# Kernel optimization log

Measured on AMD Instinct MI355X. Metric: run time of the kernel, lower is better.

Reference implementation:

```python
import math
import jax, jax.numpy as jnp
import numpy as np

B, N, C, H = 4, 1025, 768, 12
D = C // H                      # head_dim = 64
SCALE = D ** -0.5
NUM = N // 4                    # CSA block size = 256
FUSE_T = math.ceil(0.1 * (N - 1))     # 103
ENH_T = math.ceil(0.1 * (N - 1))      # 103


def _csa_mask():
    # has_cls=True: tokens 1..4*NUM get block id 0..3; cls (idx 0) gets -1 (unmasked).
    bid = (jnp.arange(N) - 1) // NUM
    same = (bid[:, None] == bid[None, :]) & (bid[:, None] >= 0) & (bid[:, None] < 4)
    return jnp.where(same, -jnp.inf, 0.0).astype(jnp.float32)  # [N, N]


def setup_inputs() -> dict:
    key = jax.random.key(0)
    kx, kq, kw, kb = jax.random.split(key, 4)
    x = jax.random.normal(kx, (B, N, C), dtype=jnp.float32)
    w_qkv = jax.random.normal(kq, (3 * C, C), dtype=jnp.float32) * 0.02  # Linear(C, 3C, bias=False)
    w_out = jax.random.normal(kw, (C, C), dtype=jnp.float32) * 0.02
    b_out = jax.random.normal(kb, (C,), dtype=jnp.float32) * 0.02
    return {"x": x, "w_qkv": w_qkv, "w_out": w_out, "b_out": b_out}


def reference(x, w_qkv, w_out, b_out):
    b, n, c = x.shape
    h, d = H, c // H
    # qkv projection + rearrange 'b n (qkv h d) -> qkv b h n d'
    qkv = (x @ w_qkv.T).reshape(b, n, 3, h, d).transpose(2, 0, 3, 1, 4)
    q, k, v = qkv[0], qkv[1], qkv[2]          # each [b, h, n, d]

    scores = jnp.einsum('bhxd,bhyd->bhxy', q, k) * SCALE + _csa_mask()
    att = jax.nn.softmax(scores, axis=-1)     # [b, h, n, n]  (dropout=0, eval)

    ctx = jnp.einsum('bhxy,bhyd->bhxd', att, v)
    out = ctx.transpose(0, 2, 1, 3).reshape(b, n, c) @ w_out.T + b_out

    # cls-attention-driven token selection
    cls_attn = att[:, :, 0, 1:].mean(axis=1)  # [b, n-1]
    _, fuse_idx = jax.lax.top_k(-cls_attn, FUSE_T)   # smallest, ascending
    _, enh_idx = jax.lax.top_k(cls_attn, ENH_T)      # largest, descending
    fuse_index = jnp.broadcast_to(fuse_idx[:, :, None], (b, FUSE_T, c))
    enhance_index = jnp.broadcast_to(enh_idx[:, :, None], (b, ENH_T, c))
    return (out, enhance_index, enh_idx, fuse_index, fuse_idx, cls_attn)
```

## Files before the change

kernel.cpp:

```cpp
#include <hip/hip_runtime.h>


#define B_  4
#define N_  1025
#define C_  768
#define H_  12
#define D_  64
#define M_TOT (B_ * N_)
#define M_PAD 4224
#define KEXP 2304
#define NPAD 1088

#define OFF_EIND 3148800
#define OFF_EIDX 3465216
#define OFF_FIND 3465628
#define OFF_FIDX 3782044
#define OFF_CLS  3782456

#define WS_F64   0
#define WS_XS    196608
#define WS_QKVB  5062656
#define WS_OUTB  7716864
#define WS_QE    8601600
#define WS_KE    11943936
#define WS_VT    15286272

#define DQ0 0
#define DMS 3072
#define DLG 39936
#define DMX 89136
#define DZ  89184
#define DMV 89232

#define SPLIT_A_ITEMS (M_PAD * 192)
#define SPLIT_B1_ITEMS (2304 * 192)
#define SPLIT_B2_ITEMS (768 * 192)
#define SPLIT_TOTAL (SPLIT_A_ITEMS + SPLIT_B1_ITEMS + SPLIT_B2_ITEMS)

typedef short s16x8 __attribute__((ext_vector_type(8)));
typedef float f32x4 __attribute__((ext_vector_type(4)));

__device__ inline unsigned short f2bf(float f) {
    unsigned u = __float_as_uint(f);
    u += 0x7FFF + ((u >> 16) & 1);
    return (unsigned short)(u >> 16);
}
__device__ inline float bf2f(unsigned short h) {
    return __uint_as_float(((unsigned)h) << 16);
}

__device__ __forceinline__ void gl2lds16(const unsigned short* g, unsigned short* l) {
    __builtin_amdgcn_global_load_lds(
        (const __attribute__((address_space(1))) unsigned int*)g,
        (__attribute__((address_space(3))) unsigned int*)l,
        16, 0, 0);
}

__device__ inline void gemm_decode(int lid, int NT, int& m, int& n) {
    int gi = lid / (8 * NT);
    int r  = lid % (8 * NT);
    int base = gi * 8;
    int gsize = (33 - base < 8) ? (33 - base) : 8;
    n = r / gsize;
    m = base + r % gsize;
}

__global__ __launch_bounds__(256) void split_all_kernel(
    const float* __restrict__ x, const float* __restrict__ w_qkv,
    const float* __restrict__ w_out,
    unsigned short* __restrict__ xs, unsigned short* __restrict__ qkvB,
    unsigned short* __restrict__ outB)
{
    int idx = blockIdx.x * 256 + threadIdx.x;
    if (idx < SPLIT_A_ITEMS) {
        int m = idx / 192, c4 = (idx - m * 192) * 4;
        ushort4 hi = make_ushort4(0,0,0,0), lo = hi;
        if (m < M_TOT) {
            float4 f = *(const float4*)&x[(size_t)m * C_ + c4];
            hi.x = f2bf(f.x); hi.y = f2bf(f.y); hi.z = f2bf(f.z); hi.w = f2bf(f.w);
            lo.x = f2bf(f.x - bf2f(hi.x)); lo.y = f2bf(f.y - bf2f(hi.y));
            lo.z = f2bf(f.z - bf2f(hi.z)); lo.w = f2bf(f.w - bf2f(hi.w));
        }
        unsigned short* d = xs + (size_t)m * KEXP + c4;
        *(ushort4*)(d)        = hi;
        *(ushort4*)(d + 768)  = hi;
        *(ushort4*)(d + 1536) = lo;
        return;
    }
    idx -= SPLIT_A_ITEMS;
    const float* src;
    unsigned short* dst;
    if (idx < SPLIT_B1_ITEMS) { src = w_qkv; dst = qkvB; }
    else { idx -= SPLIT_B1_ITEMS; if (idx >= SPLIT_B2_ITEMS) return; src = w_out; dst = outB; }
    int m = idx / 192, c4 = (idx - m * 192) * 4;
    float4 f = *(const float4*)&src[(size_t)m * C_ + c4];
    ushort4 hi, lo;
    hi.x = f2bf(f.x); hi.y = f2bf(f.y); hi.z = f2bf(f.z); hi.w = f2bf(f.w);
    lo.x = f2bf(f.x - bf2f(hi.x)); lo.y = f2bf(f.y - bf2f(hi.y));
    lo.z = f2bf(f.z - bf2f(hi.z)); lo.w = f2bf(f.w - bf2f(hi.w));
    unsigned short* d = dst + (size_t)m * KEXP + c4;
    *(ushort4*)(d)        = hi;
    *(ushort4*)(d + 768)  = lo;
    *(ushort4*)(d + 1536) = hi;
}

__global__ __launch_bounds__(256) void gemm_qkv_kernel(
    const unsigned short* __restrict__ A, const unsigned short* __restrict__ Bm,
    unsigned short* __restrict__ qe, unsigned short* __restrict__ ke,
    unsigned short* __restrict__ vtp)
{
    __shared__ unsigned short AsF[3*4096];
    __shared__ unsigned short BsF[3*4096];
    int mi, ni;
    gemm_decode(blockIdx.x, 18, mi, ni);
    const int n0 = ni * 128;
    const int m0 = mi * 128;
    const int t = threadIdx.x;
    const int lane = t & 63, wv = t >> 6;
    const int wr = wv >> 1, wc = wv & 1;
    const int q4 = lane >> 4, r = lane & 15;
    const int lrr = lane >> 2;
    const int lcc = ((lane & 3) ^ ((lane >> 3) & 3)) * 8;
    const int sw  = (q4 ^ ((r >> 1) & 3)) * 8;

    f32x4 acc[4][4];
    #pragma unroll
    for (int i = 0; i < 4; i++)
        #pragma unroll
        for (int j = 0; j < 4; j++)
            #pragma unroll
            for (int e = 0; e < 4; e++) acc[i][j][e] = 0.f;

    const unsigned short* gA = A  + (size_t)(m0 + wv*16 + lrr) * KEXP + lcc;
    const unsigned short* gB = Bm + (size_t)(n0 + wv*16 + lrr) * KEXP + lcc;

    auto STAGE = [&](int kt, int o) {
        const unsigned short* a = gA + kt * 32;
        const unsigned short* b = gB + kt * 32;
        gl2lds16(a,                       AsF + o + wv*512);
        gl2lds16(a + (size_t)64 * KEXP,   AsF + o + 2048 + wv*512);
        gl2lds16(b,                       BsF + o + wv*512);
        gl2lds16(b + (size_t)64 * KEXP,   BsF + o + 2048 + wv*512);
    };

    STAGE(0, 0);
    STAGE(1, 4096);

    int cb = 0;
    for (int it = 0; it < 72; ++it) {
        if (it + 1 < 72) asm volatile("s_waitcnt vmcnt(4)" ::: "memory");
        else             asm volatile("s_waitcnt vmcnt(0)" ::: "memory");
        __builtin_amdgcn_s_barrier();
        asm volatile("" ::: "memory");
        __builtin_amdgcn_sched_barrier(0);
        if (it + 2 < 72) {
            int nb = (cb >= 1) ? cb - 1 : cb + 2;
            STAGE(it + 2, nb * 4096);
        }
        const int cbuf = cb * 4096;
        s16x8 af[4], bfr[4];
        #pragma unroll
        for (int i = 0; i < 4; i++) {
            af[i]  = *(const s16x8*)&AsF[cbuf + (wr*64 + i*16 + r)*32 + sw];
            bfr[i] = *(const s16x8*)&BsF[cbuf + (wc*64 + i*16 + r)*32 + sw];
        }
        #pragma unroll
        for (int i = 0; i < 4; i++)
            #pragma unroll
            for (int j = 0; j < 4; j++)
                acc[i][j] = __builtin_amdgcn_mfma_f32_16x16x32_bf16(af[i], bfr[j], acc[i][j], 0, 0, 0);
        cb = (cb < 2) ? cb + 1 : 0;
    }

    const int sel = n0 / C_;
    const int off = n0 % C_;
    const float scl = (sel == 0) ? 0.125f : 1.0f;
    #pragma unroll
    for (int i = 0; i < 4; i++) {
        #pragma unroll
        for (int rr = 0; rr < 4; rr++) {
            int gm = m0 + wr*64 + i*16 + q4*4 + rr;
            if (gm < M_TOT) {
                int bb = gm / N_, n = gm - bb * N_;
                #pragma unroll
                for (int j = 0; j < 4; j++) {
                    int col = off + wc*64 + j*16 + r;
                    int h = col >> 6, d = col & 63;
                    float val = acc[i][j][rr] * scl;
                    unsigned short hi = f2bf(val);
                    unsigned short lo = f2bf(val - bf2f(hi));
                    size_t bh = (size_t)(bb*H_ + h);
                    if (sel <= 1) {
                        unsigned short* dst = (sel == 0 ? qe : ke) + (bh*NPAD + n)*128;
                        dst[d]      = hi;
                        dst[64 + d] = lo;
                    } else {
                        unsigned short* dst = vtp + bh*128*NPAD;
                        dst[(size_t)d*NPAD + n]        = hi;
                        dst[(size_t)(64 + d)*NPAD + n] = lo;
                    }
                }
            }
        }
    }
}

__global__ __launch_bounds__(256) void gemm_out_kernel(
    const unsigned short* __restrict__ A, const unsigned short* __restrict__ Bm,
    const float* __restrict__ bias, float* __restrict__ out)
{
    __shared__ unsigned short AsF[3*4096];
    __shared__ unsigned short BsF[3*4096];
    int mi, ni;
    gemm_decode(blockIdx.x, 6, mi, ni);
    const int n0 = ni * 128;
    const int m0 = mi * 128;
    const int t = threadIdx.x;
    const int lane = t & 63, wv = t >> 6;
    const int wr = wv >> 1, wc = wv & 1;
    const int q4 = lane >> 4, r = lane & 15;
    const int lrr = lane >> 2;
    const int lcc = ((lane & 3) ^ ((lane >> 3) & 3)) * 8;
    const int sw  = (q4 ^ ((r >> 1) & 3)) * 8;

    f32x4 acc[4][4];
    #pragma unroll
    for (int i = 0; i < 4; i++)
        #pragma unroll
        for (int j = 0; j < 4; j++)
            #pragma unroll
            for (int e = 0; e < 4; e++) acc[i][j][e] = 0.f;

    const unsigned short* gA = A  + (size_t)(m0 + wv*16 + lrr) * KEXP + lcc;
    const unsigned short* gB = Bm + (size_t)(n0 + wv*16 + lrr) * KEXP + lcc;

    auto STAGE = [&](int kt, int o) {
        const unsigned short* a = gA + kt * 32;
        const unsigned short* b = gB + kt * 32;
        gl2lds16(a,                       AsF + o + wv*512);
        gl2lds16(a + (size_t)64 * KEXP,   AsF + o + 2048 + wv*512);
        gl2lds16(b,                       BsF + o + wv*512);
        gl2lds16(b + (size_t)64 * KEXP,   BsF + o + 2048 + wv*512);
    };

    STAGE(0, 0);
    STAGE(1, 4096);

    int cb = 0;
    for (int it = 0; it < 72; ++it) {
        if (it + 1 < 72) asm volatile("s_waitcnt vmcnt(4)" ::: "memory");
        else             asm volatile("s_waitcnt vmcnt(0)" ::: "memory");
        __builtin_amdgcn_s_barrier();
        asm volatile("" ::: "memory");
        __builtin_amdgcn_sched_barrier(0);
        if (it + 2 < 72) {
            int nb = (cb >= 1) ? cb - 1 : cb + 2;
            STAGE(it + 2, nb * 4096);
        }
        const int cbuf = cb * 4096;
        s16x8 af[4], bfr[4];
        #pragma unroll
        for (int i = 0; i < 4; i++) {
            af[i]  = *(const s16x8*)&AsF[cbuf + (wr*64 + i*16 + r)*32 + sw];
            bfr[i] = *(const s16x8*)&BsF[cbuf + (wc*64 + i*16 + r)*32 + sw];
        }
        #pragma unroll
        for (int i = 0; i < 4; i++)
            #pragma unroll
            for (int j = 0; j < 4; j++)
                acc[i][j] = __builtin_amdgcn_mfma_f32_16x16x32_bf16(af[i], bfr[j], acc[i][j], 0, 0, 0);
        cb = (cb < 2) ? cb + 1 : 0;
    }

    #pragma unroll
    for (int i = 0; i < 4; i++) {
        #pragma unroll
        for (int rr = 0; rr < 4; rr++) {
            int gm = m0 + wr*64 + i*16 + q4*4 + rr;
            if (gm < M_TOT) {
                #pragma unroll
                for (int j = 0; j < 4; j++) {
                    int col = n0 + wc*64 + j*16 + r;
                    out[(size_t)gm * C_ + col] = acc[i][j][rr] + bias[col];
                }
            }
        }
    }
}

__global__ __launch_bounds__(256, 4) void attn_kernel(
    const unsigned short* __restrict__ qe, const unsigned short* __restrict__ ke,
    const unsigned short* __restrict__ vtp, unsigned short* __restrict__ ctxs)
{
    __shared__ unsigned short KP[64*128];
    __shared__ unsigned short VP[128*64];

    const int qt = blockIdx.x / 48;
    const int g  = blockIdx.x - qt * 48;
    const int h = g % 12, b = g / 12;
    const int t = threadIdx.x;
    const int w = t >> 6, lane = t & 63;
    const int quad = lane >> 4, r16 = lane & 15;
    const size_t bh = (size_t)(b*H_ + h);

    s16x8 ah0, ah1, al0, al1;
    {
        const unsigned short* qrow = qe + (bh*NPAD + qt*64 + w*16 + r16) * 128;
        const int q8 = quad * 8;
        ah0 = *(const s16x8*)(qrow + q8);
        ah1 = *(const s16x8*)(qrow + 32 + q8);
        al0 = *(const s16x8*)(qrow + 64 + q8);
        al1 = *(const s16x8*)(qrow + 96 + q8);
    }

    int qu;
    {
        int rlo = qt*64, rhi = min(qt*64 + 63, N_ - 1);
        if (rlo == 0) qu = -2;
        else { int b1 = (rlo-1)>>8, b2 = (rhi-1)>>8; qu = (b1==b2) ? b1 : -2; }
    }

    float m_run[4], l_run[4];
    f32x4 ctx[4];
    #pragma unroll
    for (int i = 0; i < 4; i++) {
        m_run[i] = -1e30f; l_run[i] = 0.f;
        #pragma unroll
        for (int e = 0; e < 4; e++) ctx[i][e] = 0.f;
    }

    const unsigned short* keb = ke  + (bh*NPAD) * 128;
    const unsigned short* vtb = vtp + bh*(size_t)128*NPAD;

    const int kchunk = (t & 15) ^ ((t >> 4) & 15);
    const int vchunk = (t & 7)  ^ ((t >> 3) & 7);
    const unsigned short* kg0 = keb + (size_t)(t >> 4) * 128 + kchunk * 8;
    const unsigned short* vg0 = vtb + (size_t)(t >> 3) * NPAD + vchunk * 8;

    const int s0 = (quad ^ r16) << 3;
    const int sv = (quad ^ (r16 & 7)) << 3;
    unsigned short* Pew = KP + w*16*128;

    for (int kt = 0; kt < 17; kt++) {
        if (qu >= 0 && kt > 0) {
            int clo = kt*64, chi = min(kt*64 + 63, N_ - 1);
            int b1 = (clo-1)>>8, b2 = (chi-1)>>8;
            if (b1 == b2 && b1 == qu) continue;
        }

        __syncthreads();
        {
            const unsigned short* kg = kg0 + (size_t)kt * 64 * 128;
            const unsigned short* vg = vg0 + kt * 64;
            #pragma unroll
            for (int i = 0; i < 4; i++) {
                gl2lds16(kg + i * 2048,              KP + i*2048 + w*512);
                gl2lds16(vg + (size_t)i * 32 * NPAD, VP + i*2048 + w*512);
            }
        }
        __syncthreads();

        f32x4 st[4];
        #pragma unroll
        for (int j = 0; j < 4; j++)
            #pragma unroll
            for (int e = 0; e < 4; e++) st[j][e] = 0.f;
        #pragma unroll
        for (int j = 0; j < 4; j++) {
            const unsigned short* kr = &KP[(j*16 + r16) * 128];
            s16x8 bh0 = *(const s16x8*)&kr[s0];
            s16x8 bh1 = *(const s16x8*)&kr[s0 ^ 32];
            s16x8 bl0 = *(const s16x8*)&kr[s0 ^ 64];
            s16x8 bl1 = *(const s16x8*)&kr[s0 ^ 96];
            st[j] = __builtin_amdgcn_mfma_f32_16x16x32_bf16(ah0, bh0, st[j], 0,0,0);
            st[j] = __builtin_amdgcn_mfma_f32_16x16x32_bf16(ah1, bh1, st[j], 0,0,0);
            st[j] = __builtin_amdgcn_mfma_f32_16x16x32_bf16(ah0, bl0, st[j], 0,0,0);
            st[j] = __builtin_amdgcn_mfma_f32_16x16x32_bf16(ah1, bl1, st[j], 0,0,0);
            st[j] = __builtin_amdgcn_mfma_f32_16x16x32_bf16(al0, bh0, st[j], 0,0,0);
            st[j] = __builtin_amdgcn_mfma_f32_16x16x32_bf16(al1, bh1, st[j], 0,0,0);
        }

        float pv[4][4];
        float alpha[4];
        #pragma unroll
        for (int reg = 0; reg < 4; reg++) {
            int gr = qt*64 + w*16 + quad*4 + reg;
            int qb = (gr >= 1) ? ((gr - 1) >> 8) : -1;
            float mx = -1e30f;
            float vv[4];
            #pragma unroll
            for (int j = 0; j < 4; j++) {
                int gc = kt*64 + j*16 + r16;
                bool ok = (gr < N_) && (gc < N_) &&
                          !((gr >= 1) && (gc >= 1) && (((gc - 1) >> 8) == qb));
                vv[j] = ok ? st[j][reg] : -1e30f;
                mx = fmaxf(mx, vv[j]);
            }
            mx = fmaxf(mx, __shfl_xor(mx, 1));
            mx = fmaxf(mx, __shfl_xor(mx, 2));
            mx = fmaxf(mx, __shfl_xor(mx, 4));
            mx = fmaxf(mx, __shfl_xor(mx, 8));
            float mnew = fmaxf(m_run[reg], mx);
            alpha[reg] = __expf(m_run[reg] - mnew);
            m_run[reg] = mnew;
            float ps = 0.f;
            #pragma unroll
            for (int j = 0; j < 4; j++) {
                float pp = (vv[j] > -1e29f) ? __expf(vv[j] - mnew) : 0.f;
                pv[reg][j] = pp; ps += pp;
            }
            ps += __shfl_xor(ps, 1);
            ps += __shfl_xor(ps, 2);
            ps += __shfl_xor(ps, 4);
            ps += __shfl_xor(ps, 8);
            l_run[reg] = l_run[reg] * alpha[reg] + ps;
        }

        __syncthreads();

        #pragma unroll
        for (int reg = 0; reg < 4; reg++) {
            int lrow = quad*4 + reg;
            #pragma unroll
            for (int j = 0; j < 4; j++) {
                float pp = pv[reg][j];
                unsigned short ph = f2bf(pp);
                unsigned short pl = f2bf(pp - bf2f(ph));
                int colh = j*16 + r16;
                int coll = 64 + colh;
                Pew[lrow*128 + (((colh >> 3) ^ lrow) << 3) + (colh & 7)] = ph;
                Pew[lrow*128 + (((coll >> 3) ^ lrow) << 3) + (coll & 7)] = pl;
            }
        }

        #pragma unroll
        for (int nj = 0; nj < 4; nj++)
            #pragma unroll
            for (int reg = 0; reg < 4; reg++)
                ctx[nj][reg] *= alpha[reg];

        {
            const unsigned short* pr = &Pew[r16 * 128];
            s16x8 ph0 = *(const s16x8*)&pr[s0];
            s16x8 ph1 = *(const s16x8*)&pr[s0 ^ 32];
            s16x8 pl0 = *(const s16x8*)&pr[s0 ^ 64];
            s16x8 pl1 = *(const s16x8*)&pr[s0 ^ 96];
            #pragma unroll
            for (int nj = 0; nj < 4; nj++) {
                const unsigned short* vh = &VP[(nj*16 + r16) * 64];
                const unsigned short* vl = &VP[(64 + nj*16 + r16) * 64];
                s16x8 vh0 = *(const s16x8*)&vh[sv];
                s16x8 vh1 = *(const s16x8*)&vh[sv ^ 32];
                s16x8 vl0 = *(const s16x8*)&vl[sv];
                s16x8 vl1 = *(const s16x8*)&vl[sv ^ 32];
                ctx[nj] = __builtin_amdgcn_mfma_f32_16x16x32_bf16(ph0, vh0, ctx[nj], 0,0,0);
                ctx[nj] = __builtin_amdgcn_mfma_f32_16x16x32_bf16(ph1, vh1, ctx[nj], 0,0,0);
                ctx[nj] = __builtin_amdgcn_mfma_f32_16x16x32_bf16(ph0, vl0, ctx[nj], 0,0,0);
                ctx[nj] = __builtin_amdgcn_mfma_f32_16x16x32_bf16(ph1, vl1, ctx[nj], 0,0,0);
                ctx[nj] = __builtin_amdgcn_mfma_f32_16x16x32_bf16(pl0, vh0, ctx[nj], 0,0,0);
                ctx[nj] = __builtin_amdgcn_mfma_f32_16x16x32_bf16(pl1, vh1, ctx[nj], 0,0,0);
            }
        }
    }

    #pragma unroll
    for (int reg = 0; reg < 4; reg++) {
        int gr = qt*64 + w*16 + quad*4 + reg;
        if (gr < N_) {
            float inv = 1.0f / l_run[reg];
            size_t row = (size_t)(b*N_ + gr) * KEXP;
            #pragma unroll
            for (int nj = 0; nj < 4; nj++) {
                float val = ctx[nj][reg] * inv;
                unsigned short hi = f2bf(val);
                unsigned short lo = f2bf(val - bf2f(hi));
                int c = h*64 + nj*16 + r16;
                ctxs[row + c]        = hi;
                ctxs[row + 768 + c]  = hi;
                ctxs[row + 1536 + c] = lo;
            }
        }
    }
}

__global__ __launch_bounds__(256) void cls_q0_kernel(
    const float* __restrict__ x, const float* __restrict__ w_qkv,
    double* __restrict__ dws)
{
    const int t = threadIdx.x;
    const int wg = blockIdx.x * 4 + (t >> 6);
    const int lane = t & 63;
    const int b = wg / 768, rem = wg - b * 768;
    const float* x0 = x + (size_t)b * N_ * C_;
    const float* wr = w_qkv + (size_t)rem * C_;
    double s = 0.0;
    #pragma unroll
    for (int i = 0; i < 12; i++) {
        int c = lane + i*64;
        s += (double)x0[c] * (double)wr[c];
    }
    #pragma unroll
    for (int o = 1; o < 64; o <<= 1) s += __shfl_xor(s, o);
    if (lane == 0) dws[DQ0 + wg] = s * 0.125;
}

__global__ __launch_bounds__(256) void cls_ms_kernel(
    const float* __restrict__ w_qkv, double* __restrict__ dws)
{
    __shared__ double q0s[64];
    const int t = threadIdx.x;
    const int c = blockIdx.x * 256 + t;
    const int h = blockIdx.y, b = blockIdx.z;
    if (t < 64) q0s[t] = dws[DQ0 + (b*H_ + h)*64 + t];
    __syncthreads();
    const float* wk = w_qkv + (size_t)(C_ + h*64) * C_ + c;
    double s = 0.0;
    #pragma unroll 8
    for (int d = 0; d < 64; d++) s += q0s[d] * (double)wk[(size_t)d * C_];
    dws[DMS + ((size_t)(b*H_ + h))*768 + c] = s;
}

__global__ __launch_bounds__(256) void cls_logits_kernel(
    const float* __restrict__ x, double* __restrict__ dws)
{
    __shared__ double xs[768];
    const int j = blockIdx.x, b = blockIdx.y;
    const int t = threadIdx.x;
    const int w = t >> 6, lane = t & 63;
    const float* xr = x + ((size_t)b * N_ + j) * C_;
    for (int c = t; c < C_; c += 256) xs[c] = (double)xr[c];
    __syncthreads();
    for (int hh = 0; hh < 3; hh++) {
        int h = w + hh * 4;
        const double* ms = dws + DMS + ((size_t)(b*H_ + h))*768;
        double s = 0.0;
        #pragma unroll
        for (int i = 0; i < 12; i++) {
            int c = lane + i*64;
            s += xs[c] * ms[c];
        }
        #pragma unroll
        for (int o = 1; o < 64; o <<= 1) s += __shfl_xor(s, o);
        if (lane == 0) dws[DLG + ((size_t)(b*H_ + h))*1025 + j] = s;
    }
}

__global__ __launch_bounds__(256) void cls_reduce_kernel(
    const double* __restrict__ dwsr, double* __restrict__ dws)
{
    __shared__ double red[256];
    const int h = blockIdx.x, b = blockIdx.y;
    const int t = threadIdx.x;
    const double* lg = dwsr + DLG + ((size_t)(b*H_ + h))*1025;
    double mloc = -1e300;
    for (int j = t; j < N_; j += 256) mloc = fmax(mloc, lg[j]);
    red[t] = mloc; __syncthreads();
    for (int o = 128; o > 0; o >>= 1) {
        if (t < o) red[t] = fmax(red[t], red[t+o]);
        __syncthreads();
    }
    double mx = red[0]; __syncthreads();
    double sloc = 0.0;
    for (int j = t; j < N_; j += 256) sloc += exp(lg[j] - mx);
    red[t] = sloc; __syncthreads();
    for (int o = 128; o > 0; o >>= 1) {
        if (t < o) red[t] += red[t+o];
        __syncthreads();
    }
    if (t == 0) {
        dws[DMX + b*H_ + h] = mx;
        dws[DZ  + b*H_ + h] = red[0];
    }
}

__global__ __launch_bounds__(256) void cls_score_kernel(
    const double* __restrict__ dwsr, double* __restrict__ dws,
    float* __restrict__ out)
{
    const int idx = blockIdx.x * 256 + threadIdx.x;
    const int b = idx >> 10, t = idx & 1023;
    double s = 0.0;
    #pragma unroll
    for (int h = 0; h < H_; h++) {
        double mx = dwsr[DMX + b*H_ + h];
        double Z  = dwsr[DZ  + b*H_ + h];
        double lg = dwsr[DLG + ((size_t)(b*H_ + h))*1025 + (t + 1)];
        s += exp(lg - mx) / Z;
    }
    s *= (1.0 / 12.0);
    dws[DMV + idx] = s;
    out[OFF_CLS + (size_t)b*1024 + t] = (float)s;
}

__global__ __launch_bounds__(256) void cls_rank_kernel(
    const double* __restrict__ dws, float* __restrict__ out)
{
    __shared__ double mv[1024];
    const int q = blockIdx.x, b = blockIdx.y;
    const int tid = threadIdx.x;
    for (int i = tid; i < 1024; i += 256) mv[i] = dws[DMV + b*1024 + i];
    __syncthreads();
    const int t = q*256 + tid;
    const double v = mv[t];
    int cd = 0, ca = 0;
    #pragma unroll 8
    for (int j = 0; j < 1024; j++) {
        double u = mv[j];
        bool tie = (u == v) && (j < t);
        cd += (u > v) || tie;
        ca += (u < v) || tie;
    }
    if (cd < 103) out[OFF_EIDX + (size_t)b*103 + cd] = (float)t;
    if (ca < 103) out[OFF_FIDX + (size_t)b*103 + ca] = (float)t;
}

__global__ __launch_bounds__(256) void cls_fill_kernel(float* __restrict__ out)
{
    const int PER = 103 * 192;
    int idx = blockIdx.x * 256 + threadIdx.x;
    if (idx >= 2 * 4 * PER) return;
    int sel = idx / (4 * PER);
    int r   = idx - sel * 4 * PER;
    int b   = r / PER;
    int rem = r - b * PER;
    int e   = rem / 192;
    int c4  = (rem - e * 192) * 4;
    float val = out[(sel ? OFF_FIDX : OFF_EIDX) + (size_t)b*103 + e];
    float* dst = out + (sel ? OFF_FIND : OFF_EIND) + ((size_t)b*103 + e)*768 + c4;
    *(float4*)dst = make_float4(val, val, val, val);
}

extern "C" void kernel_launch(void* const* d_in, const int* in_sizes, int n_in,
                              void* d_out, int out_size, void* d_ws, size_t ws_size,
                              hipStream_t stream)
{
    const float* x     = (const float*)d_in[0];
    const float* w_qkv = (const float*)d_in[1];
    const float* w_out = (const float*)d_in[2];
    const float* b_out = (const float*)d_in[3];
    float* out = (float*)d_out;
    float* ws  = (float*)d_ws;

    double* dws = (double*)(ws + WS_F64);
    unsigned short* xs   = (unsigned short*)(ws + WS_XS);
    unsigned short* qkvB = (unsigned short*)(ws + WS_QKVB);
    unsigned short* outB = (unsigned short*)(ws + WS_OUTB);
    unsigned short* qe   = (unsigned short*)(ws + WS_QE);
    unsigned short* ke   = (unsigned short*)(ws + WS_KE);
    unsigned short* vtp  = (unsigned short*)(ws + WS_VT);

    split_all_kernel<<<(SPLIT_TOTAL + 255)/256, 256, 0, stream>>>(
        x, w_qkv, w_out, xs, qkvB, outB);

    gemm_qkv_kernel<<<594, 256, 0, stream>>>(xs, qkvB, qe, ke, vtp);
    attn_kernel<<<816, 256, 0, stream>>>(qe, ke, vtp, xs);

    cls_q0_kernel<<<768, 256, 0, stream>>>(x, w_qkv, dws);
    cls_ms_kernel<<<dim3(3, H_, B_), 256, 0, stream>>>(w_qkv, dws);
    cls_logits_kernel<<<dim3(N_, B_), 256, 0, stream>>>(x, dws);
    cls_reduce_kernel<<<dim3(H_, B_), 256, 0, stream>>>(dws, dws);
    cls_score_kernel<<<16, 256, 0, stream>>>(dws, dws, out);
    cls_rank_kernel<<<dim3(4, B_), 256, 0, stream>>>(dws, out);
    cls_fill_kernel<<<618, 256, 0, stream>>>(out);

    gemm_out_kernel<<<198, 256, 0, stream>>>(xs, outB, b_out, out);
}
```

Baseline: 376.2 us.

## Fold the CLS-attention side chain into the main-path kernel launches

The four CLS-score kernels (q0, ms, logits, reduce) are merged into the split, QKV GEMM, attention and output-GEMM launches as extra blocks that branch off by blockIdx. Each side stage rides on a main-path kernel whose stream predecessor already produced its inputs. This removes four launches and their inter-kernel gaps, and lets the small double-precision work fill idle CUs next to the GEMM and attention blocks. In exchange, the fused kernels take on their partners' register and LDS budgets, and the extra blocks may compete with or trail the main tiles.

```diff
diff --git a/kernel.cpp b/kernel.cpp
--- a/kernel.cpp
+++ b/kernel.cpp
@@ -36,6 +36,7 @@
 #define SPLIT_B1_ITEMS (2304 * 192)
 #define SPLIT_B2_ITEMS (768 * 192)
 #define SPLIT_TOTAL (SPLIT_A_ITEMS + SPLIT_B1_ITEMS + SPLIT_B2_ITEMS)
+#define SPLIT_BLOCKS ((SPLIT_TOTAL + 255) / 256)
 
 typedef short s16x8 __attribute__((ext_vector_type(8)));
 typedef float f32x4 __attribute__((ext_vector_type(4)));
@@ -65,12 +66,30 @@
     m = base + r % gsize;
 }
 
-__global__ __launch_bounds__(256) void split_all_kernel(
+__global__ __launch_bounds__(256) void fused_split_q0_kernel(
     const float* __restrict__ x, const float* __restrict__ w_qkv,
     const float* __restrict__ w_out,
     unsigned short* __restrict__ xs, unsigned short* __restrict__ qkvB,
-    unsigned short* __restrict__ outB)
-{
+    unsigned short* __restrict__ outB, double* __restrict__ dws)
+{
+    if (blockIdx.x >= SPLIT_BLOCKS) {
+        const int t = threadIdx.x;
+        const int wg = (blockIdx.x - SPLIT_BLOCKS) * 4 + (t >> 6);
+        const int lane = t & 63;
+        const int b = wg / 768, rem = wg - b * 768;
+        const float* x0 = x + (size_t)b * N_ * C_;
+        const float* wr = w_qkv + (size_t)rem * C_;
+        double s = 0.0;
+        #pragma unroll
+        for (int i = 0; i < 12; i++) {
+            int c = lane + i*64;
+            s += (double)x0[c] * (double)wr[c];
+        }
+        #pragma unroll
+        for (int o = 1; o < 64; o <<= 1) s += __shfl_xor(s, o);
+        if (lane == 0) dws[DQ0 + wg] = s * 0.125;
+        return;
+    }
     int idx = blockIdx.x * 256 + threadIdx.x;
     if (idx < SPLIT_A_ITEMS) {
         int m = idx / 192, c4 = (idx - m * 192) * 4;
@@ -104,13 +123,33 @@
     *(ushort4*)(d + 1536) = hi;
 }
 
-__global__ __launch_bounds__(256) void gemm_qkv_kernel(
+__global__ __launch_bounds__(256) void fused_gemm_qkv_ms_kernel(
     const unsigned short* __restrict__ A, const unsigned short* __restrict__ Bm,
     unsigned short* __restrict__ qe, unsigned short* __restrict__ ke,
-    unsigned short* __restrict__ vtp)
+    unsigned short* __restrict__ vtp,
+    const float* __restrict__ w_qkv, double* __restrict__ dws)
 {
     __shared__ unsigned short AsF[3*4096];
     __shared__ unsigned short BsF[3*4096];
+
+    if (blockIdx.x >= 594) {
+        double* q0s = (double*)AsF;
+        const int lid = blockIdx.x - 594;
+        const int cb = lid % 3;
+        const int h  = (lid / 3) % 12;
+        const int b  = lid / 36;
+        const int t = threadIdx.x;
+        const int c = cb * 256 + t;
+        if (t < 64) q0s[t] = dws[DQ0 + (b*H_ + h)*64 + t];
+        __syncthreads();
+        const float* wk = w_qkv + (size_t)(C_ + h*64) * C_ + c;
+        double s = 0.0;
+        #pragma unroll 8
+        for (int d = 0; d < 64; d++) s += q0s[d] * (double)wk[(size_t)d * C_];
+        dws[DMS + ((size_t)(b*H_ + h))*768 + c] = s;
+        return;
+    }
+
     int mi, ni;
     gemm_decode(blockIdx.x, 18, mi, ni);
     const int n0 = ni * 128;
@@ -205,95 +244,38 @@
     }
 }
 
-__global__ __launch_bounds__(256) void gemm_out_kernel(
-    const unsigned short* __restrict__ A, const unsigned short* __restrict__ Bm,
-    const float* __restrict__ bias, float* __restrict__ out)
-{
-    __shared__ unsigned short AsF[3*4096];
-    __shared__ unsigned short BsF[3*4096];
-    int mi, ni;
-    gemm_decode(blockIdx.x, 6, mi, ni);
-    const int n0 = ni * 128;
-    const int m0 = mi * 128;
-    const int t = threadIdx.x;
-    const int lane = t & 63, wv = t >> 6;
-    const int wr = wv >> 1, wc = wv & 1;
-    const int q4 = lane >> 4, r = lane & 15;
-    const int lrr = lane >> 2;
-    const int lcc = ((lane & 3) ^ ((lane >> 3) & 3)) * 8;
-    const int sw  = (q4 ^ ((r >> 1) & 3)) * 8;
-
-    f32x4 acc[4][4];
-    #pragma unroll
-    for (int i = 0; i < 4; i++)
-        #pragma unroll
-        for (int j = 0; j < 4; j++)
-            #pragma unroll
-            for (int e = 0; e < 4; e++) acc[i][j][e] = 0.f;
-
-    const unsigned short* gA = A  + (size_t)(m0 + wv*16 + lrr) * KEXP + lcc;
-    const unsigned short* gB = Bm + (size_t)(n0 + wv*16 + lrr) * KEXP + lcc;
-
-    auto STAGE = [&](int kt, int o) {
-        const unsigned short* a = gA + kt * 32;
-        const unsigned short* b = gB + kt * 32;
-        gl2lds16(a,                       AsF + o + wv*512);
-        gl2lds16(a + (size_t)64 * KEXP,   AsF + o + 2048 + wv*512);
-        gl2lds16(b,                       BsF + o + wv*512);
-        gl2lds16(b + (size_t)64 * KEXP,   BsF + o + 2048 + wv*512);
-    };
-
-    STAGE(0, 0);
-    STAGE(1, 4096);
-
-    int cb = 0;
-    for (int it = 0; it < 72; ++it) {
-        if (it + 1 < 72) asm volatile("s_waitcnt vmcnt(4)" ::: "memory");
-        else             asm volatile("s_waitcnt vmcnt(0)" ::: "memory");
-        __builtin_amdgcn_s_barrier();
-        asm volatile("" ::: "memory");
-        __builtin_amdgcn_sched_barrier(0);
-        if (it + 2 < 72) {
-            int nb = (cb >= 1) ? cb - 1 : cb + 2;
-            STAGE(it + 2, nb * 4096);
-        }
-        const int cbuf = cb * 4096;
-        s16x8 af[4], bfr[4];
-        #pragma unroll
-        for (int i = 0; i < 4; i++) {
-            af[i]  = *(const s16x8*)&AsF[cbuf + (wr*64 + i*16 + r)*32 + sw];
-            bfr[i] = *(const s16x8*)&BsF[cbuf + (wc*64 + i*16 + r)*32 + sw];
-        }
-        #pragma unroll
-        for (int i = 0; i < 4; i++)
-            #pragma unroll
-            for (int j = 0; j < 4; j++)
-                acc[i][j] = __builtin_amdgcn_mfma_f32_16x16x32_bf16(af[i], bfr[j], acc[i][j], 0, 0, 0);
-        cb = (cb < 2) ? cb + 1 : 0;
-    }
-
-    #pragma unroll
-    for (int i = 0; i < 4; i++) {
-        #pragma unroll
-        for (int rr = 0; rr < 4; rr++) {
-            int gm = m0 + wr*64 + i*16 + q4*4 + rr;
-            if (gm < M_TOT) {
-                #pragma unroll
-                for (int j = 0; j < 4; j++) {
-                    int col = n0 + wc*64 + j*16 + r;
-                    out[(size_t)gm * C_ + col] = acc[i][j][rr] + bias[col];
-                }
-            }
-        }
-    }
-}
-
-__global__ __launch_bounds__(256, 4) void attn_kernel(
+__global__ __launch_bounds__(256, 4) void fused_attn_logits_kernel(
     const unsigned short* __restrict__ qe, const unsigned short* __restrict__ ke,
-    const unsigned short* __restrict__ vtp, unsigned short* __restrict__ ctxs)
+    const unsigned short* __restrict__ vtp, unsigned short* __restrict__ ctxs,
+    const float* __restrict__ x, double* __restrict__ dws)
 {
     __shared__ unsigned short KP[64*128];
     __shared__ unsigned short VP[128*64];
+
+    if (blockIdx.x >= 816) {
+        double* xsd = (double*)KP;
+        const int lid = blockIdx.x - 816;
+        const int j = lid % 1025, b = lid / 1025;
+        const int t = threadIdx.x;
+        const int w = t >> 6, lane = t & 63;
+        const float* xr = x + ((size_t)b * N_ + j) * C_;
+        for (int c = t; c < C_; c += 256) xsd[c] = (double)xr[c];
+        __syncthreads();
+        for (int hh = 0; hh < 3; hh++) {
+            int h = w + hh * 4;
+            const double* ms = dws + DMS + ((size_t)(b*H_ + h))*768;
+            double s = 0.0;
+            #pragma unroll
+            for (int i = 0; i < 12; i++) {
+                int c = lane + i*64;
+                s += xsd[c] * ms[c];
+            }
+            #pragma unroll
+            for (int o = 1; o < 64; o <<= 1) s += __shfl_xor(s, o);
+            if (lane == 0) dws[DLG + ((size_t)(b*H_ + h))*1025 + j] = s;
+        }
+        return;
+    }
 
     const int qt = blockIdx.x / 48;
     const int g  = blockIdx.x - qt * 48;
@@ -483,93 +465,116 @@
     }
 }
 
-__global__ __launch_bounds__(256) void cls_q0_kernel(
-    const float* __restrict__ x, const float* __restrict__ w_qkv,
+__global__ __launch_bounds__(256) void fused_gemm_out_reduce_kernel(
+    const unsigned short* __restrict__ A, const unsigned short* __restrict__ Bm,
+    const float* __restrict__ bias, float* __restrict__ out,
     double* __restrict__ dws)
 {
+    __shared__ unsigned short AsF[3*4096];
+    __shared__ unsigned short BsF[3*4096];
+
+    if (blockIdx.x >= 198) {
+        double* red = (double*)AsF;
+        const int lid = blockIdx.x - 198;
+        const int h = lid % 12, b = lid / 12;
+        const int t = threadIdx.x;
+        const double* lg = dws + DLG + ((size_t)(b*H_ + h))*1025;
+        double mloc = -1e300;
+        for (int j = t; j < N_; j += 256) mloc = fmax(mloc, lg[j]);
+        red[t] = mloc; __syncthreads();
+        for (int o = 128; o > 0; o >>= 1) {
+            if (t < o) red[t] = fmax(red[t], red[t+o]);
+            __syncthreads();
+        }
+        double mx = red[0]; __syncthreads();
+        double sloc = 0.0;
+        for (int j = t; j < N_; j += 256) sloc += exp(lg[j] - mx);
+        red[t] = sloc; __syncthreads();
+        for (int o = 128; o > 0; o >>= 1) {
+            if (t < o) red[t] += red[t+o];
+            __syncthreads();
+        }
+        if (t == 0) {
+            dws[DMX + b*H_ + h] = mx;
+            dws[DZ  + b*H_ + h] = red[0];
+        }
+        return;
+    }
+
+    int mi, ni;
+    gemm_decode(blockIdx.x, 6, mi, ni);
+    const int n0 = ni * 128;
+    const int m0 = mi * 128;
     const int t = threadIdx.x;
-    const int wg = blockIdx.x * 4 + (t >> 6);
-    const int lane = t & 63;
-    const int b = wg / 768, rem = wg - b * 768;
-    const float* x0 = x + (size_t)b * N_ * C_;
-    const float* wr = w_qkv + (size_t)rem * C_;
-    double s = 0.0;
+    const int lane = t & 63, wv = t >> 6;
+    const int wr = wv >> 1, wc = wv & 1;
+    const int q4 = lane >> 4, r = lane & 15;
+    const int lrr = lane >> 2;
+    const int lcc = ((lane & 3) ^ ((lane >> 3) & 3)) * 8;
+    const int sw  = (q4 ^ ((r >> 1) & 3)) * 8;
+
+    f32x4 acc[4][4];
     #pragma unroll
-    for (int i = 0; i < 12; i++) {
-        int c = lane + i*64;
-        s += (double)x0[c] * (double)wr[c];
-    }
+    for (int i = 0; i < 4; i++)
+        #pragma unroll
+        for (int j = 0; j < 4; j++)
+            #pragma unroll
+            for (int e = 0; e < 4; e++) acc[i][j][e] = 0.f;
+
+    const unsigned short* gA = A  + (size_t)(m0 + wv*16 + lrr) * KEXP + lcc;
+    const unsigned short* gB = Bm + (size_t)(n0 + wv*16 + lrr) * KEXP + lcc;
+
+    auto STAGE = [&](int kt, int o) {
+        const unsigned short* a = gA + kt * 32;
+        const unsigned short* b = gB + kt * 32;
+        gl2lds16(a,                       AsF + o + wv*512);
+        gl2lds16(a + (size_t)64 * KEXP,   AsF + o + 2048 + wv*512);
+        gl2lds16(b,                       BsF + o + wv*512);
+        gl2lds16(b + (size_t)64 * KEXP,   BsF + o + 2048 + wv*512);
+    };
+
+    STAGE(0, 0);
+    STAGE(1, 4096);
+
+    int cb = 0;
+    for (int it = 0; it < 72; ++it) {
+        if (it + 1 < 72) asm volatile("s_waitcnt vmcnt(4)" ::: "memory");
+        else             asm volatile("s_waitcnt vmcnt(0)" ::: "memory");
+        __builtin_amdgcn_s_barrier();
+        asm volatile("" ::: "memory");
+        __builtin_amdgcn_sched_barrier(0);
+        if (it + 2 < 72) {
+            int nb = (cb >= 1) ? cb - 1 : cb + 2;
+            STAGE(it + 2, nb * 4096);
+        }
+        const int cbuf = cb * 4096;
+        s16x8 af[4], bfr[4];
+        #pragma unroll
+        for (int i = 0; i < 4; i++) {
+            af[i]  = *(const s16x8*)&AsF[cbuf + (wr*64 + i*16 + r)*32 + sw];
+            bfr[i] = *(const s16x8*)&BsF[cbuf + (wc*64 + i*16 + r)*32 + sw];
+        }
+        #pragma unroll
+        for (int i = 0; i < 4; i++)
+            #pragma unroll
+            for (int j = 0; j < 4; j++)
+                acc[i][j] = __builtin_amdgcn_mfma_f32_16x16x32_bf16(af[i], bfr[j], acc[i][j], 0, 0, 0);
+        cb = (cb < 2) ? cb + 1 : 0;
+    }
+
     #pragma unroll
-    for (int o = 1; o < 64; o <<= 1) s += __shfl_xor(s, o);
-    if (lane == 0) dws[DQ0 + wg] = s * 0.125;
-}
-
-__global__ __launch_bounds__(256) void cls_ms_kernel(
-    const float* __restrict__ w_qkv, double* __restrict__ dws)
-{
-    __shared__ double q0s[64];
-    const int t = threadIdx.x;
-    const int c = blockIdx.x * 256 + t;
-    const int h = blockIdx.y, b = blockIdx.z;
-    if (t < 64) q0s[t] = dws[DQ0 + (b*H_ + h)*64 + t];
-    __syncthreads();
-    const float* wk = w_qkv + (size_t)(C_ + h*64) * C_ + c;
-    double s = 0.0;
-    #pragma unroll 8
-    for (int d = 0; d < 64; d++) s += q0s[d] * (double)wk[(size_t)d * C_];
-    dws[DMS + ((size_t)(b*H_ + h))*768 + c] = s;
-}
-
-__global__ __launch_bounds__(256) void cls_logits_kernel(
-    const float* __restrict__ x, double* __restrict__ dws)
-{
-    __shared__ double xs[768];
-    const int j = blockIdx.x, b = blockIdx.y;
-    const int t = threadIdx.x;
-    const int w = t >> 6, lane = t & 63;
-    const float* xr = x + ((size_t)b * N_ + j) * C_;
-    for (int c = t; c < C_; c += 256) xs[c] = (double)xr[c];
-    __syncthreads();
-    for (int hh = 0; hh < 3; hh++) {
-        int h = w + hh * 4;
-        const double* ms = dws + DMS + ((size_t)(b*H_ + h))*768;
-        double s = 0.0;
-        #pragma unroll
-        for (int i = 0; i < 12; i++) {
-            int c = lane + i*64;
-            s += xs[c] * ms[c];
-        }
-        #pragma unroll
-        for (int o = 1; o < 64; o <<= 1) s += __shfl_xor(s, o);
-        if (lane == 0) dws[DLG + ((size_t)(b*H_ + h))*1025 + j] = s;
-    }
-}
-
-__global__ __launch_bounds__(256) void cls_reduce_kernel(
-    const double* __restrict__ dwsr, double* __restrict__ dws)
-{
-    __shared__ double red[256];
-    const int h = blockIdx.x, b = blockIdx.y;
-    const int t = threadIdx.x;
-    const double* lg = dwsr + DLG + ((size_t)(b*H_ + h))*1025;
-    double mloc = -1e300;
-    for (int j = t; j < N_; j += 256) mloc = fmax(mloc, lg[j]);
-    red[t] = mloc; __syncthreads();
-    for (int o = 128; o > 0; o >>= 1) {
-        if (t < o) red[t] = fmax(red[t], red[t+o]);
-        __syncthreads();
-    }
-    double mx = red[0]; __syncthreads();
-    double sloc = 0.0;
-    for (int j = t; j < N_; j += 256) sloc += exp(lg[j] - mx);
-    red[t] = sloc; __syncthreads();
-    for (int o = 128; o > 0; o >>= 1) {
-        if (t < o) red[t] += red[t+o];
-        __syncthreads();
-    }
-    if (t == 0) {
-        dws[DMX + b*H_ + h] = mx;
-        dws[DZ  + b*H_ + h] = red[0];
+    for (int i = 0; i < 4; i++) {
+        #pragma unroll
+        for (int rr = 0; rr < 4; rr++) {
+            int gm = m0 + wr*64 + i*16 + q4*4 + rr;
+            if (gm < M_TOT) {
+                #pragma unroll
+                for (int j = 0; j < 4; j++) {
+                    int col = n0 + wc*64 + j*16 + r;
+                    out[(size_t)gm * C_ + col] = acc[i][j][rr] + bias[col];
+                }
+            }
+        }
     }
 }
 
@@ -649,19 +654,19 @@
     unsigned short* ke   = (unsigned short*)(ws + WS_KE);
     unsigned short* vtp  = (unsigned short*)(ws + WS_VT);
 
-    split_all_kernel<<<(SPLIT_TOTAL + 255)/256, 256, 0, stream>>>(
-        x, w_qkv, w_out, xs, qkvB, outB);
-
-    gemm_qkv_kernel<<<594, 256, 0, stream>>>(xs, qkvB, qe, ke, vtp);
-    attn_kernel<<<816, 256, 0, stream>>>(qe, ke, vtp, xs);
-
-    cls_q0_kernel<<<768, 256, 0, stream>>>(x, w_qkv, dws);
-    cls_ms_kernel<<<dim3(3, H_, B_), 256, 0, stream>>>(w_qkv, dws);
-    cls_logits_kernel<<<dim3(N_, B_), 256, 0, stream>>>(x, dws);
-    cls_reduce_kernel<<<dim3(H_, B_), 256, 0, stream>>>(dws, dws);
+    fused_split_q0_kernel<<<SPLIT_BLOCKS + 768, 256, 0, stream>>>(
+        x, w_qkv, w_out, xs, qkvB, outB, dws);
+
+    fused_gemm_qkv_ms_kernel<<<594 + 144, 256, 0, stream>>>(
+        xs, qkvB, qe, ke, vtp, w_qkv, dws);
+
+    fused_attn_logits_kernel<<<816 + 4100, 256, 0, stream>>>(
+        qe, ke, vtp, xs, x, dws);
+
+    fused_gemm_out_reduce_kernel<<<198 + 48, 256, 0, stream>>>(
+        xs, outB, b_out, out, dws);
+
     cls_score_kernel<<<16, 256, 0, stream>>>(dws, dws, out);
     cls_rank_kernel<<<dim3(4, B_), 256, 0, stream>>>(dws, out);
     cls_fill_kernel<<<618, 256, 0, stream>>>(out);
-
-    gemm_out_kernel<<<198, 256, 0, stream>>>(xs, outB, b_out, out);
-}
+}
```

New measurement: 348.9 us. 7.2% less time.
